# Performance work log

Measured on AMD Instinct MI355X. Metric: run time of the kernel, lower is better.

## Reference

```python
import jax, jax.numpy as jnp
import numpy as np

DIM = 1024
DIM_QK = 1024
DIM_V = 1024
H = 16
SCALE = 1.0 / (DIM_QK ** 0.5)  # NOTE: module scales by sqrt(dim_qk), not sqrt(head_dim)


def setup_inputs() -> dict:
    key = jax.random.key(0)
    ks = jax.random.split(key, 12)
    B, S = 2, 2048
    q = jax.random.normal(ks[0], (B, S, DIM), jnp.float32)
    k = jax.random.normal(ks[1], (B, S, DIM), jnp.float32)
    v = jax.random.normal(ks[2], (B, S, DIM), jnp.float32)
    mask = jax.random.randint(ks[3], (B, 1, S, S), 0, 2) > 0  # True = masked
    s = 1.0 / np.sqrt(DIM)
    Wq = jax.random.uniform(ks[4], (DIM_QK, DIM), jnp.float32, -s, s)
    bq = jax.random.uniform(ks[5], (DIM_QK,), jnp.float32, -s, s)
    Wk = jax.random.uniform(ks[6], (DIM_QK, DIM), jnp.float32, -s, s)
    bk = jax.random.uniform(ks[7], (DIM_QK,), jnp.float32, -s, s)
    Wv = jax.random.uniform(ks[8], (DIM_V, DIM), jnp.float32, -s, s)
    bv = jax.random.uniform(ks[9], (DIM_V,), jnp.float32, -s, s)
    Wo = jax.random.uniform(ks[10], (DIM_V, DIM), jnp.float32, -s, s)
    bo = jax.random.uniform(ks[11], (DIM_V,), jnp.float32, -s, s)
    return {"q": q, "k": k, "v": v, "mask": mask,
            "Wq": Wq, "bq": bq, "Wk": Wk, "bk": bk,
            "Wv": Wv, "bv": bv, "Wo": Wo, "bo": bo}


def reference(q, k, v, mask, Wq, bq, Wk, bk, Wv, bv, Wo, bo):
    B, Sq, _ = q.shape
    Skv = k.shape[1]
    # projections (torch Linear: x @ W.T + b)
    qh = (q @ Wq.T + bq).reshape(B, Sq, H, DIM_QK // H).transpose(0, 2, 1, 3)   # [B,H,Sq,dk]
    kh = (k @ Wk.T + bk).reshape(B, Skv, H, DIM_QK // H).transpose(0, 2, 1, 3)  # [B,H,Skv,dk]
    vh = (v @ Wv.T + bv).reshape(B, Skv, H, DIM_V // H).transpose(0, 2, 1, 3)   # [B,H,Skv,dv]
    attn = jnp.einsum('bhqd,bhkd->bhqk', qh, kh) * SCALE
    attn = jnp.where(mask, jnp.float32(-1e20), attn)
    attn = jax.nn.softmax(attn, axis=-1)
    # dropout is identity in eval / p=0
    out = jnp.einsum('bhqk,bhkd->bhqd', attn, vh)            # [B,H,Sq,dv]
    out = out.transpose(0, 2, 1, 3).reshape(B, Sq, DIM_V)
    return out @ Wo.T + bo
```

## Files before the change

### kernel.cpp

```cpp
#include <hip/hip_runtime.h>
#include <hip/hip_bf16.h>

typedef __attribute__((ext_vector_type(8))) __bf16 bf16x8;
typedef __attribute__((ext_vector_type(4))) float f32x4;
typedef __attribute__((ext_vector_type(4))) unsigned int uint4v;
typedef __attribute__((ext_vector_type(2))) unsigned int uint2v;

#define S_LEN 2048
#define DIM_  1024
#define HDIM  64
#define SCALE2 0.045084441f
#define QK_STR 80
#define V_STR  72
#define P_STR  80

#define EXP2F(x) __builtin_amdgcn_exp2f(x)

__device__ __forceinline__ void async_copy16(const void* gp, void* lp) {
  __builtin_amdgcn_global_load_lds(
      (const __attribute__((address_space(1))) unsigned int*)gp,
      (__attribute__((address_space(3))) unsigned int*)lp, 16, 0, 0);
}

__device__ __forceinline__ unsigned f2bf_u(float f) {
  unsigned u = __builtin_bit_cast(unsigned, f);
  return (u + 0x7FFFu + ((u >> 16) & 1u)) >> 16;
}
__device__ __forceinline__ unsigned pack2(float a, float b) {
  return f2bf_u(a) | (f2bf_u(b) << 16);
}

__global__ __launch_bounds__(256) void cvt_kernel(
    const float* __restrict__ s0, const float* __restrict__ s1, const float* __restrict__ s2,
    const float* __restrict__ s3, const float* __restrict__ s4, const float* __restrict__ s5,
    const float* __restrict__ s6,
    __hip_bfloat16* __restrict__ d0, __hip_bfloat16* __restrict__ d1, __hip_bfloat16* __restrict__ d2,
    __hip_bfloat16* __restrict__ d3, __hip_bfloat16* __restrict__ d4, __hip_bfloat16* __restrict__ d5,
    __hip_bfloat16* __restrict__ d6)
{
  const float* srcs[7] = {s0, s1, s2, s3, s4, s5, s6};
  __hip_bfloat16* dsts[7] = {d0, d1, d2, d3, d4, d5, d6};
  const int sizes[7] = {4194304, 4194304, 4194304, 1048576, 1048576, 1048576, 1048576};
  int rg = blockIdx.y;
  int base = (blockIdx.x * 256 + threadIdx.x) * 8;
  if (base >= sizes[rg]) return;
  const float* s = srcs[rg] + base;
  f32x4 a = *(const f32x4*)s;
  f32x4 b = *(const f32x4*)(s + 4);
  uint4v o;
  o.x = pack2(a[0], a[1]); o.y = pack2(a[2], a[3]);
  o.z = pack2(b[0], b[1]); o.w = pack2(b[2], b[3]);
  *(uint4v*)(dsts[rg] + base) = o;
}

__global__ __launch_bounds__(256) void maskbits_kernel(
    const int* __restrict__ mask, unsigned long long* __restrict__ bits)
{
  int w = (blockIdx.x * 256 + threadIdx.x) >> 6;
  int lane = threadIdx.x & 63;
  int m = mask[(size_t)w * 64 + lane];
  unsigned long long bal = __ballot(m != 0);
  if (lane == 0) bits[w] = bal;
}

__global__ __launch_bounds__(256) void qkv_gemm_kernel(
    const __hip_bfloat16* __restrict__ xq, const __hip_bfloat16* __restrict__ xk,
    const __hip_bfloat16* __restrict__ xv,
    const __hip_bfloat16* __restrict__ Wq, const float* __restrict__ bq,
    const __hip_bfloat16* __restrict__ Wk, const float* __restrict__ bk,
    const __hip_bfloat16* __restrict__ Wv, const float* __restrict__ bv,
    __hip_bfloat16* __restrict__ Q, __hip_bfloat16* __restrict__ Kk,
    __hip_bfloat16* __restrict__ VT)
{
  const __hip_bfloat16 *X, *W; const float* bias;
  if (blockIdx.z == 0)      { X = xq; W = Wq; bias = bq; }
  else if (blockIdx.z == 1) { X = xk; W = Wk; bias = bk; }
  else                      { X = xv; W = Wv; bias = bv; }

  constexpr int K = 1024, N = 1024;
  __shared__ alignas(16) __hip_bfloat16 As[128 * 32];
  __shared__ alignas(16) __hip_bfloat16 Bs[128 * 32];
  const int tid  = threadIdx.x;
  const int lane = tid & 63;
  const int wave = tid >> 6;
  const int t    = lane & 15;
  const int quad = lane >> 4;
  const int wm   = wave >> 1;
  const int wn   = wave & 1;
  const int m0   = blockIdx.x * 128;
  const int n0   = blockIdx.y * 128;

  f32x4 acc[4][4] = {};

  for (int k0 = 0; k0 < K; k0 += 32) {
    __syncthreads();
#pragma unroll
    for (int r = 0; r < 2; ++r) {
      int c   = r * 256 + tid;
      int row = c >> 2;
      int col = (c & 3) * 8;
      async_copy16(&X[(size_t)(m0 + row) * K + k0 + col], &As[c * 8]);
      async_copy16(&W[(size_t)(n0 + row) * K + k0 + col], &Bs[c * 8]);
    }
    __syncthreads();
    bf16x8 a[4], b[4];
#pragma unroll
    for (int i = 0; i < 4; ++i)
      a[i] = *(const bf16x8*)&As[(wm * 64 + i * 16 + t) * 32 + quad * 8];
#pragma unroll
    for (int j = 0; j < 4; ++j)
      b[j] = *(const bf16x8*)&Bs[(wn * 64 + j * 16 + t) * 32 + quad * 8];
#pragma unroll
    for (int i = 0; i < 4; ++i)
#pragma unroll
      for (int j = 0; j < 4; ++j)
        acc[i][j] = __builtin_amdgcn_mfma_f32_16x16x32_bf16(a[i], b[j], acc[i][j], 0, 0, 0);
  }

  float bj[4];
#pragma unroll
  for (int j = 0; j < 4; ++j)
    bj[j] = bias[n0 + wn * 64 + j * 16 + t];

  if (blockIdx.z == 2) {
#pragma unroll
    for (int i = 0; i < 4; ++i)
#pragma unroll
      for (int j = 0; j < 4; ++j) {
        int m = m0 + wm * 64 + i * 16 + quad * 4;
        int n = n0 + wn * 64 + j * 16 + t;
        int bb = m >> 11, kv = m & 2047;
        int hh = n >> 6,  dv = n & 63;
        uint2v o;
        o.x = pack2(acc[i][j][0] + bj[j], acc[i][j][1] + bj[j]);
        o.y = pack2(acc[i][j][2] + bj[j], acc[i][j][3] + bj[j]);
        *(uint2v*)&VT[(size_t)(((bb * 16 + hh) * 64) + dv) * 2048 + kv] = o;
      }
  } else {
    __hip_bfloat16* Out = (blockIdx.z == 0) ? Q : Kk;
#pragma unroll
    for (int i = 0; i < 4; ++i)
#pragma unroll
      for (int j = 0; j < 4; ++j)
#pragma unroll
        for (int r = 0; r < 4; ++r) {
          int m = m0 + wm * 64 + i * 16 + quad * 4 + r;
          int n = n0 + wn * 64 + j * 16 + t;
          Out[(size_t)m * N + n] = __float2bfloat16(acc[i][j][r] + bj[j]);
        }
  }
}

__global__ __launch_bounds__(256) void proj_gemm_kernel(
    const __hip_bfloat16* __restrict__ X, const __hip_bfloat16* __restrict__ W,
    const float* __restrict__ bias, float* __restrict__ Out)
{
  constexpr int K = 1024, N = 1024;
  __shared__ alignas(16) __hip_bfloat16 As[128 * 32];
  __shared__ alignas(16) __hip_bfloat16 Bs[128 * 32];
  const int tid  = threadIdx.x;
  const int lane = tid & 63;
  const int wave = tid >> 6;
  const int t    = lane & 15;
  const int quad = lane >> 4;
  const int wm   = wave >> 1;
  const int wn   = wave & 1;
  const int m0   = blockIdx.x * 128;
  const int n0   = blockIdx.y * 128;

  f32x4 acc[4][4] = {};

  for (int k0 = 0; k0 < K; k0 += 32) {
    __syncthreads();
#pragma unroll
    for (int r = 0; r < 2; ++r) {
      int c   = r * 256 + tid;
      int row = c >> 2;
      int col = (c & 3) * 8;
      async_copy16(&X[(size_t)(m0 + row) * K + k0 + col], &As[c * 8]);
      async_copy16(&W[(size_t)(n0 + row) * K + k0 + col], &Bs[c * 8]);
    }
    __syncthreads();
    bf16x8 a[4], b[4];
#pragma unroll
    for (int i = 0; i < 4; ++i)
      a[i] = *(const bf16x8*)&As[(wm * 64 + i * 16 + t) * 32 + quad * 8];
#pragma unroll
    for (int j = 0; j < 4; ++j)
      b[j] = *(const bf16x8*)&Bs[(wn * 64 + j * 16 + t) * 32 + quad * 8];
#pragma unroll
    for (int i = 0; i < 4; ++i)
#pragma unroll
      for (int j = 0; j < 4; ++j)
        acc[i][j] = __builtin_amdgcn_mfma_f32_16x16x32_bf16(a[i], b[j], acc[i][j], 0, 0, 0);
  }

  float bj[4];
#pragma unroll
  for (int j = 0; j < 4; ++j)
    bj[j] = bias[n0 + wn * 64 + j * 16 + t];
#pragma unroll
  for (int i = 0; i < 4; ++i)
#pragma unroll
    for (int j = 0; j < 4; ++j)
#pragma unroll
      for (int r = 0; r < 4; ++r) {
        int m = m0 + wm * 64 + i * 16 + quad * 4 + r;
        int n = n0 + wn * 64 + j * 16 + t;
        Out[(size_t)m * N + n] = acc[i][j][r] + bj[j];
      }
}

__global__ __launch_bounds__(256) void attn_kernel(
    const __hip_bfloat16* __restrict__ Qb,
    const __hip_bfloat16* __restrict__ Kb,
    const __hip_bfloat16* __restrict__ VT,
    const unsigned long long* __restrict__ mbits,
    __hip_bfloat16* __restrict__ Ob)
{
  const int bid = blockIdx.x;
  const int qt = bid & 31;
  const int h  = (bid >> 5) & 15;
  const int b  = bid >> 9;
  const int qb = qt * 64;

  __shared__ alignas(16) __hip_bfloat16 Qs[64 * QK_STR];
  __shared__ alignas(16) __hip_bfloat16 Ks[64 * QK_STR];
  __shared__ alignas(16) __hip_bfloat16 Vt[64 * V_STR];
  __shared__ alignas(16) __hip_bfloat16 Ps[64 * P_STR];

  const int tid  = threadIdx.x;
  const int lane = tid & 63;
  const int wave = tid >> 6;
  const int t    = lane & 15;
  const int quad = lane >> 4;

#pragma unroll
  for (int r = 0; r < 2; ++r) {
    int c = r * 256 + tid;
    int row = c >> 3, d0 = (c & 7) * 8;
    uint4 raw = *(const uint4*)&Qb[((size_t)(b * S_LEN + qb + row)) * DIM_ + h * HDIM + d0];
    *(uint4*)&Qs[row * QK_STR + d0] = raw;
  }
  __syncthreads();

  bf16x8 qf[2];
#pragma unroll
  for (int ks = 0; ks < 2; ++ks)
    qf[ks] = *(const bf16x8*)&Qs[(wave * 16 + t) * QK_STR + ks * 32 + quad * 8];

  float m_i = -3.0e38f;
  float l_i = 0.f;
  f32x4 o[4] = {};

  const int qg = qb + wave * 16 + t;
  const size_t vtbase = (size_t)((b * 16 + h) * 64) * 2048;
  const size_t mbase = ((size_t)b * S_LEN + qg) * 32;

  for (int kvt = 0; kvt < 32; ++kvt) {
    const int kvb = kvt * 64;
    unsigned long long mw = mbits[mbase + kvt];
    __syncthreads();
#pragma unroll
    for (int r = 0; r < 2; ++r) {
      int c = r * 256 + tid;
      int row = c >> 3, d0 = (c & 7) * 8;
      uint4 kraw = *(const uint4*)&Kb[((size_t)(b * S_LEN + kvb + row)) * DIM_ + h * HDIM + d0];
      *(uint4*)&Ks[row * QK_STR + d0] = kraw;
      uint4 vraw = *(const uint4*)&VT[vtbase + (size_t)row * 2048 + kvb + d0];
      *(uint4*)&Vt[row * V_STR + d0] = vraw;
    }
    __syncthreads();

    f32x4 s4[4];
#pragma unroll
    for (int i = 0; i < 4; ++i) {
      f32x4 z = {};
      bf16x8 a0 = *(const bf16x8*)&Ks[(i * 16 + t) * QK_STR + quad * 8];
      z = __builtin_amdgcn_mfma_f32_16x16x32_bf16(a0, qf[0], z, 0, 0, 0);
      bf16x8 a1 = *(const bf16x8*)&Ks[(i * 16 + t) * QK_STR + 32 + quad * 8];
      z = __builtin_amdgcn_mfma_f32_16x16x32_bf16(a1, qf[1], z, 0, 0, 0);
      s4[i] = z;
    }

    float p[4][4];
    float mx = -3.0e38f;
#pragma unroll
    for (int i = 0; i < 4; ++i) {
      unsigned mq = (unsigned)((mw >> (i * 16 + quad * 4)) & 0xFull);
#pragma unroll
      for (int r = 0; r < 4; ++r) {
        float v = ((mq >> r) & 1u) ? -1e20f : s4[i][r] * SCALE2;
        p[i][r] = v;
        mx = fmaxf(mx, v);
      }
    }
    mx = fmaxf(mx, __shfl_xor(mx, 16, 64));
    mx = fmaxf(mx, __shfl_xor(mx, 32, 64));
    float m_new = fmaxf(m_i, mx);
    float alpha = EXP2F(m_i - m_new);
    float sum = 0.f;
#pragma unroll
    for (int i = 0; i < 4; ++i)
#pragma unroll
      for (int r = 0; r < 4; ++r) {
        float e = EXP2F(p[i][r] - m_new);
        p[i][r] = e;
        sum += e;
      }
    sum += __shfl_xor(sum, 16, 64);
    sum += __shfl_xor(sum, 32, 64);
    l_i = alpha * l_i + sum;
    m_i = m_new;

    float alr[4];
#pragma unroll
    for (int r = 0; r < 4; ++r)
      alr[r] = __shfl(alpha, quad * 4 + r, 64);
#pragma unroll
    for (int n = 0; n < 4; ++n)
#pragma unroll
      for (int r = 0; r < 4; ++r)
        o[n][r] *= alr[r];

#pragma unroll
    for (int i = 0; i < 4; ++i) {
      uint2v pk;
      pk.x = pack2(p[i][0], p[i][1]);
      pk.y = pack2(p[i][2], p[i][3]);
      *(uint2v*)&Ps[(wave * 16 + t) * P_STR + i * 16 + quad * 4] = pk;
    }

#pragma unroll
    for (int ks = 0; ks < 2; ++ks) {
      bf16x8 pa = *(const bf16x8*)&Ps[(wave * 16 + t) * P_STR + ks * 32 + quad * 8];
#pragma unroll
      for (int n = 0; n < 4; ++n) {
        bf16x8 vb = *(const bf16x8*)&Vt[(n * 16 + t) * V_STR + ks * 32 + quad * 8];
        o[n] = __builtin_amdgcn_mfma_f32_16x16x32_bf16(pa, vb, o[n], 0, 0, 0);
      }
    }
  }

  float lr[4];
#pragma unroll
  for (int r = 0; r < 4; ++r)
    lr[r] = __shfl(l_i, quad * 4 + r, 64);
#pragma unroll
  for (int n = 0; n < 4; ++n)
#pragma unroll
    for (int r = 0; r < 4; ++r) {
      int q2 = qb + wave * 16 + quad * 4 + r;
      int col = h * HDIM + n * 16 + t;
      Ob[((size_t)b * S_LEN + q2) * DIM_ + col] = __float2bfloat16(o[n][r] / lr[r]);
    }
}

extern "C" void kernel_launch(void* const* d_in, const int* in_sizes, int n_in,
                              void* d_out, int out_size, void* d_ws, size_t ws_size,
                              hipStream_t stream) {
  const float* q  = (const float*)d_in[0];
  const float* k  = (const float*)d_in[1];
  const float* v  = (const float*)d_in[2];
  const int*   mk = (const int*)d_in[3];
  const float* Wq = (const float*)d_in[4];
  const float* bq = (const float*)d_in[5];
  const float* Wk = (const float*)d_in[6];
  const float* bk = (const float*)d_in[7];
  const float* Wv = (const float*)d_in[8];
  const float* bv = (const float*)d_in[9];
  const float* Wo = (const float*)d_in[10];
  const float* bo = (const float*)d_in[11];
  float* out = (float*)d_out;

  char* ws = (char*)d_ws;
  const size_t MB = 1024 * 1024;
  __hip_bfloat16* Qb  = (__hip_bfloat16*)(ws);
  __hip_bfloat16* Kb  = (__hip_bfloat16*)(ws + 8  * MB);
  __hip_bfloat16* VTb = (__hip_bfloat16*)(ws + 16 * MB);
  __hip_bfloat16* Ob  = (__hip_bfloat16*)(ws + 24 * MB);
  __hip_bfloat16* xqb = (__hip_bfloat16*)(ws + 32 * MB);
  __hip_bfloat16* xkb = (__hip_bfloat16*)(ws + 40 * MB);
  __hip_bfloat16* xvb = (__hip_bfloat16*)(ws + 48 * MB);
  __hip_bfloat16* Wqb = (__hip_bfloat16*)(ws + 56 * MB);
  __hip_bfloat16* Wkb = (__hip_bfloat16*)(ws + 58 * MB);
  __hip_bfloat16* Wvb = (__hip_bfloat16*)(ws + 60 * MB);
  __hip_bfloat16* Wob = (__hip_bfloat16*)(ws + 62 * MB);
  unsigned long long* mbits = (unsigned long long*)(ws + 64 * MB);

  cvt_kernel<<<dim3(2048, 7), 256, 0, stream>>>(q, k, v, Wq, Wk, Wv, Wo,
                                                xqb, xkb, xvb, Wqb, Wkb, Wvb, Wob);
  maskbits_kernel<<<dim3(32768), 256, 0, stream>>>(mk, mbits);
  qkv_gemm_kernel<<<dim3(32, 8, 3), 256, 0, stream>>>(xqb, xkb, xvb,
                                                      Wqb, bq, Wkb, bk, Wvb, bv,
                                                      Qb, Kb, VTb);
  attn_kernel<<<dim3(1024), 256, 0, stream>>>(Qb, Kb, VTb, mbits, Ob);
  proj_gemm_kernel<<<dim3(32, 8), 256, 0, stream>>>(Ob, Wob, bo, out);
}
```

Baseline: 322.1 us.

## Keep P in registers for PV MFMA, fold scale into Q, swizzle GEMM blocks

The attention kernel stops writing the softmax probabilities to LDS. It feeds them from registers into a transposed 16x16x16 bf16 MFMA with V as the A operand, which removes the per-row alpha and l shuffles. The softmax scale is folded into the Q projection epilogue, so the per-score multiply goes away. The output is staged through LDS to allow 16-byte coalesced global stores, and both GEMMs use a grouped block swizzle for better L2 reuse. The trade-off is a lower-K MFMA shape and Q being rounded to bf16 after scaling.

```diff
diff --git a/kernel.cpp b/kernel.cpp
--- a/kernel.cpp
+++ b/kernel.cpp
@@ -2,6 +2,7 @@
 #include <hip/hip_bf16.h>
 
 typedef __attribute__((ext_vector_type(8))) __bf16 bf16x8;
+typedef __attribute__((ext_vector_type(4))) short short4v;
 typedef __attribute__((ext_vector_type(4))) float f32x4;
 typedef __attribute__((ext_vector_type(4))) unsigned int uint4v;
 typedef __attribute__((ext_vector_type(2))) unsigned int uint2v;
@@ -12,7 +13,6 @@
 #define SCALE2 0.045084441f
 #define QK_STR 80
 #define V_STR  72
-#define P_STR  80
 
 #define EXP2F(x) __builtin_amdgcn_exp2f(x)
 
@@ -63,6 +63,14 @@
   if (lane == 0) bits[w] = bal;
 }
 
+__device__ __forceinline__ void swz(int r, int& m0, int& n0) {
+  int g  = r >> 6;
+  int yy = (r >> 3) & 7;
+  int xl = r & 7;
+  m0 = (g * 8 + xl) * 128;
+  n0 = yy * 128;
+}
+
 __global__ __launch_bounds__(256) void qkv_gemm_kernel(
     const __hip_bfloat16* __restrict__ xq, const __hip_bfloat16* __restrict__ xk,
     const __hip_bfloat16* __restrict__ xv,
@@ -87,8 +95,8 @@
   const int quad = lane >> 4;
   const int wm   = wave >> 1;
   const int wn   = wave & 1;
-  const int m0   = blockIdx.x * 128;
-  const int n0   = blockIdx.y * 128;
+  int m0, n0;
+  swz(blockIdx.x, m0, n0);
 
   f32x4 acc[4][4] = {};
 
@@ -137,7 +145,9 @@
         *(uint2v*)&VT[(size_t)(((bb * 16 + hh) * 64) + dv) * 2048 + kv] = o;
       }
   } else {
-    __hip_bfloat16* Out = (blockIdx.z == 0) ? Q : Kk;
+    const bool isq = (blockIdx.z == 0);
+    __hip_bfloat16* Out = isq ? Q : Kk;
+    const float sc = isq ? SCALE2 : 1.0f;
 #pragma unroll
     for (int i = 0; i < 4; ++i)
 #pragma unroll
@@ -146,7 +156,7 @@
         for (int r = 0; r < 4; ++r) {
           int m = m0 + wm * 64 + i * 16 + quad * 4 + r;
           int n = n0 + wn * 64 + j * 16 + t;
-          Out[(size_t)m * N + n] = __float2bfloat16(acc[i][j][r] + bj[j]);
+          Out[(size_t)m * N + n] = __float2bfloat16((acc[i][j][r] + bj[j]) * sc);
         }
   }
 }
@@ -165,8 +175,8 @@
   const int quad = lane >> 4;
   const int wm   = wave >> 1;
   const int wn   = wave & 1;
-  const int m0   = blockIdx.x * 128;
-  const int n0   = blockIdx.y * 128;
+  int m0, n0;
+  swz(blockIdx.x, m0, n0);
 
   f32x4 acc[4][4] = {};
 
@@ -227,7 +237,6 @@
   __shared__ alignas(16) __hip_bfloat16 Qs[64 * QK_STR];
   __shared__ alignas(16) __hip_bfloat16 Ks[64 * QK_STR];
   __shared__ alignas(16) __hip_bfloat16 Vt[64 * V_STR];
-  __shared__ alignas(16) __hip_bfloat16 Ps[64 * P_STR];
 
   const int tid  = threadIdx.x;
   const int lane = tid & 63;
@@ -290,7 +299,7 @@
       unsigned mq = (unsigned)((mw >> (i * 16 + quad * 4)) & 0xFull);
 #pragma unroll
       for (int r = 0; r < 4; ++r) {
-        float v = ((mq >> r) & 1u) ? -1e20f : s4[i][r] * SCALE2;
+        float v = ((mq >> r) & 1u) ? -1e20f : s4[i][r];
         p[i][r] = v;
         mx = fmaxf(mx, v);
       }
@@ -313,47 +322,50 @@
     l_i = alpha * l_i + sum;
     m_i = m_new;
 
-    float alr[4];
-#pragma unroll
-    for (int r = 0; r < 4; ++r)
-      alr[r] = __shfl(alpha, quad * 4 + r, 64);
 #pragma unroll
     for (int n = 0; n < 4; ++n)
 #pragma unroll
       for (int r = 0; r < 4; ++r)
-        o[n][r] *= alr[r];
-
-#pragma unroll
-    for (int i = 0; i < 4; ++i) {
+        o[n][r] *= alpha;
+
+    short4v pf[4];
+#pragma unroll
+    for (int j = 0; j < 4; ++j) {
       uint2v pk;
-      pk.x = pack2(p[i][0], p[i][1]);
-      pk.y = pack2(p[i][2], p[i][3]);
-      *(uint2v*)&Ps[(wave * 16 + t) * P_STR + i * 16 + quad * 4] = pk;
-    }
-
-#pragma unroll
-    for (int ks = 0; ks < 2; ++ks) {
-      bf16x8 pa = *(const bf16x8*)&Ps[(wave * 16 + t) * P_STR + ks * 32 + quad * 8];
+      pk.x = pack2(p[j][0], p[j][1]);
+      pk.y = pack2(p[j][2], p[j][3]);
+      pf[j] = __builtin_bit_cast(short4v, pk);
+    }
+
+#pragma unroll
+    for (int j = 0; j < 4; ++j)
 #pragma unroll
       for (int n = 0; n < 4; ++n) {
-        bf16x8 vb = *(const bf16x8*)&Vt[(n * 16 + t) * V_STR + ks * 32 + quad * 8];
-        o[n] = __builtin_amdgcn_mfma_f32_16x16x32_bf16(pa, vb, o[n], 0, 0, 0);
+        short4v va = *(const short4v*)&Vt[(n * 16 + t) * V_STR + j * 16 + quad * 4];
+        o[n] = __builtin_amdgcn_mfma_f32_16x16x16bf16_1k(va, pf[j], o[n], 0, 0, 0);
       }
-    }
-  }
-
-  float lr[4];
-#pragma unroll
-  for (int r = 0; r < 4; ++r)
-    lr[r] = __shfl(l_i, quad * 4 + r, 64);
-#pragma unroll
-  for (int n = 0; n < 4; ++n)
-#pragma unroll
-    for (int r = 0; r < 4; ++r) {
-      int q2 = qb + wave * 16 + quad * 4 + r;
-      int col = h * HDIM + n * 16 + t;
-      Ob[((size_t)b * S_LEN + q2) * DIM_ + col] = __float2bfloat16(o[n][r] / lr[r]);
-    }
+  }
+
+  float rl = 1.0f / l_i;
+  __hip_bfloat16* Ts = Qs;
+  __syncthreads();
+#pragma unroll
+  for (int n = 0; n < 4; ++n) {
+    uint2v pk;
+    pk.x = pack2(o[n][0] * rl, o[n][1] * rl);
+    pk.y = pack2(o[n][2] * rl, o[n][3] * rl);
+    *(uint2v*)&Ts[(wave * 16 + t) * V_STR + n * 16 + quad * 4] = pk;
+  }
+  __syncthreads();
+  {
+    int row = tid >> 2;
+    int d0  = (tid & 3) * 16;
+    uint4 x0 = *(const uint4*)&Ts[row * V_STR + d0];
+    uint4 x1 = *(const uint4*)&Ts[row * V_STR + d0 + 8];
+    __hip_bfloat16* dst = &Ob[((size_t)(b * S_LEN + qb + row)) * DIM_ + h * HDIM + d0];
+    *(uint4*)dst = x0;
+    *(uint4*)(dst + 8) = x1;
+  }
 }
 
 extern "C" void kernel_launch(void* const* d_in, const int* in_sizes, int n_in,
@@ -391,9 +403,9 @@
   cvt_kernel<<<dim3(2048, 7), 256, 0, stream>>>(q, k, v, Wq, Wk, Wv, Wo,
                                                 xqb, xkb, xvb, Wqb, Wkb, Wvb, Wob);
   maskbits_kernel<<<dim3(32768), 256, 0, stream>>>(mk, mbits);
-  qkv_gemm_kernel<<<dim3(32, 8, 3), 256, 0, stream>>>(xqb, xkb, xvb,
-                                                      Wqb, bq, Wkb, bk, Wvb, bv,
-                                                      Qb, Kb, VTb);
+  qkv_gemm_kernel<<<dim3(256, 1, 3), 256, 0, stream>>>(xqb, xkb, xvb,
+                                                       Wqb, bq, Wkb, bk, Wvb, bv,
+                                                       Qb, Kb, VTb);
   attn_kernel<<<dim3(1024), 256, 0, stream>>>(Qb, Kb, VTb, mbits, Ob);
-  proj_gemm_kernel<<<dim3(32, 8), 256, 0, stream>>>(Ob, Wob, bo, out);
-}
+  proj_gemm_kernel<<<dim3(256), 256, 0, stream>>>(Ob, Wob, bo, out);
+}
```

Measured after the change: 303.9 us. 5.7% less time.
